# Optimization experiments

Measured on AMD Instinct MI355X. Metric: run time of the kernel, lower is better.

Reference implementation:

```python
import jax, jax.numpy as jnp
import numpy as np

KS = (3, 3)   # kernel_size
ST = (1, 1)   # stride
PD = (1, 1)   # padding
EPS = 1e-5


def unfold(x):
    """im2col matching torch.nn.Unfold: [B,C,H,W] -> [B, C*kh*kw, L] with (c,kh,kw) channel order, L row-major."""
    kh, kw = KS; sh, sw = ST; ph, pw = PD
    x = jnp.pad(x, ((0, 0), (0, 0), (ph, ph), (pw, pw)))
    B, C, H, W = x.shape
    Ho = (H - kh) // sh + 1
    Wo = (W - kw) // sw + 1
    I = (jnp.arange(Ho) * sh)[:, None, None, None] + jnp.arange(kh)[None, :, None, None]
    J = (jnp.arange(Wo) * sw)[None, None, :, None] + jnp.arange(kw)[None, None, None, :]
    p = x[:, :, I, J]  # [B, C, Ho, kh, Wo, kw]
    return p.transpose(0, 1, 3, 5, 2, 4).reshape(B, C * kh * kw, Ho * Wo)


def fold(cols, x_shape):
    """torch.nn.Fold is exactly the adjoint of Unfold (overlap-add)."""
    _, vjp = jax.vjp(unfold, jnp.zeros(x_shape, cols.dtype))
    return vjp(cols)[0]


def setup_inputs() -> dict:
    key = jax.random.key(0)
    k = jax.random.split(key, 6)
    B, C, H, W = 16, 64, 64, 64
    Cout, K = 64, KS[0] * KS[1]
    return {
        "x_mag": jax.random.uniform(k[0], (B, C, H, W), jnp.float32),
        "x_ang": jax.random.normal(k[1], (B, C, H, W), jnp.float32),
        "w_mag": jax.random.uniform(k[2], (C, K), jnp.float32),
        "w_ang": jax.random.uniform(k[3], (C, K), jnp.float32),
        "w1": jax.random.uniform(k[4], (C, K), jnp.float32),
        "w2": jax.random.uniform(k[5], (Cout, C), jnp.float32),
    }


def reference(x_mag, x_ang, w_mag, w_ang, w1, w2):
    B, C, H, W = x_mag.shape
    K = KS[0] * KS[1]
    Cout = w2.shape[0]
    Ho = (H + 2 * PD[0] - KS[0]) // ST[0] + 1
    Wo = (W + 2 * PD[1] - KS[1]) // ST[1] + 1

    # outer layer: unfold, mix with normalized weights, fold back (overlap-add)
    nws_mag = w_mag ** 2 / jnp.sum(w_mag ** 2)   # _normalize_weights_squared
    nw_ang = w_ang / jnp.sum(w_ang ** 2)         # _normalize_weights
    cm = unfold(x_mag).reshape(B, C, K, -1) + nws_mag[None, :, :, None]
    ca = unfold(x_ang).reshape(B, C, K, -1) * nw_ang[None, :, :, None]
    fm = fold(cm.reshape(B, C * K, -1), (B, C, H, W))
    fa = fold(ca.reshape(B, C * K, -1), (B, C, H, W))

    # helper: second unfold + weighted Frechet-mean reduction
    tbm = unfold(fm).reshape(B, C, K, -1)  # [B,C,K,L]
    tba = unfold(fa).reshape(B, C, K, -1)
    wmm1 = w1 ** 2 / jnp.sum(w1 ** 2, axis=1, keepdims=True)  # row-normalized
    wmm2 = w2 ** 2 / jnp.sum(w2 ** 2, axis=1, keepdims=True)
    wma1 = w1 ** 2 / jnp.sum(w1 ** 2)                          # globally normalized
    wma2 = w2 ** 2 / jnp.sum(w2 ** 2)

    m1 = jnp.einsum('bckl,ck->bcl', jnp.log(tbm + EPS), wmm1)
    out_mag = jnp.exp(jnp.einsum('bcl,oc->bol', m1, wmm2)).reshape(B, Cout, Ho, Wo)
    a1 = jnp.einsum('bckl,ck->bcl', tba, wma1)
    out_ang = jnp.einsum('bcl,oc->bol', a1, wma2).reshape(B, Cout, Ho, Wo)

    # from_polar -> stack (real, imag) on axis 1
    return jnp.stack([out_mag * jnp.cos(out_ang), out_mag * jnp.sin(out_ang)], axis=1)
```

## Files before the change

### kernel.cpp

```cpp
#include <hip/hip_runtime.h>
#include <math.h>

#define NB 16
#define NC 64
#define NL 4096
#define EPSF 1e-5f
#define LOG_EPSF -11.512925464970229f
#define CC 4
#define NCHUNK 16

#define WS_W2T   0
#define WS_RHO   4096
#define WS_SMAG  4160
#define WS_TANG  4736
#define WS_IS12  5312

typedef float f32x2 __attribute__((ext_vector_type(2)));

#define FMA16(ACC, MV, W) \
  (ACC)[0].x = fmaf((MV).x,(W).x,(ACC)[0].x); (ACC)[0].y = fmaf((MV).y,(W).x,(ACC)[0].y); \
  (ACC)[0].z = fmaf((MV).z,(W).x,(ACC)[0].z); (ACC)[0].w = fmaf((MV).w,(W).x,(ACC)[0].w); \
  (ACC)[1].x = fmaf((MV).x,(W).y,(ACC)[1].x); (ACC)[1].y = fmaf((MV).y,(W).y,(ACC)[1].y); \
  (ACC)[1].z = fmaf((MV).z,(W).y,(ACC)[1].z); (ACC)[1].w = fmaf((MV).w,(W).y,(ACC)[1].w); \
  (ACC)[2].x = fmaf((MV).x,(W).z,(ACC)[2].x); (ACC)[2].y = fmaf((MV).y,(W).z,(ACC)[2].y); \
  (ACC)[2].z = fmaf((MV).z,(W).z,(ACC)[2].z); (ACC)[2].w = fmaf((MV).w,(W).z,(ACC)[2].w); \
  (ACC)[3].x = fmaf((MV).x,(W).w,(ACC)[3].x); (ACC)[3].y = fmaf((MV).y,(W).w,(ACC)[3].y); \
  (ACC)[3].z = fmaf((MV).z,(W).w,(ACC)[3].z); (ACC)[3].w = fmaf((MV).w,(W).w,(ACC)[3].w);

__global__ __launch_bounds__(256) void prep_kernel(
    const float* __restrict__ wm, const float* __restrict__ wa,
    const float* __restrict__ w1, const float* __restrict__ w2,
    float* __restrict__ ws)
{
    __shared__ float r2s[64];
    __shared__ float red[3][4];
    const int tid  = threadIdx.x;
    const int lane = tid & 63;
    const int wv   = tid >> 6;

    if (tid < 64) {
        float s = 0.f;
        for (int c = 0; c < 64; ++c) { float v = w2[tid * 64 + c]; s = fmaf(v, v, s); }
        r2s[tid] = s;
    }
    float p0 = 0.f, p1 = 0.f, p2 = 0.f;
    {
        float v;
        v = wm[tid]; p0 += v * v;  v = wm[tid + 256]; p0 += v * v;
        v = wa[tid]; p1 += v * v;  v = wa[tid + 256]; p1 += v * v;
        v = w1[tid]; p2 += v * v;  v = w1[tid + 256]; p2 += v * v;
        if (tid < 64) {
            v = wm[tid + 512]; p0 += v * v;
            v = wa[tid + 512]; p1 += v * v;
            v = w1[tid + 512]; p2 += v * v;
        }
    }
    #pragma unroll
    for (int s = 32; s; s >>= 1) {
        p0 += __shfl_down(p0, s); p1 += __shfl_down(p1, s); p2 += __shfl_down(p2, s);
    }
    if (lane == 0) { red[0][wv] = p0; red[1][wv] = p1; red[2][wv] = p2; }
    __syncthreads();
    const float s_wm2 = red[0][0] + red[0][1] + red[0][2] + red[0][3];
    const float s_wa2 = red[1][0] + red[1][1] + red[1][2] + red[1][3];
    const float s_w12 = red[2][0] + red[2][1] + red[2][2] + red[2][3];

    const int c0 = blockIdx.x * 4;
    {
        int c = c0 + (tid >> 6), o = tid & 63;
        float v = w2[o * 64 + c];
        ws[WS_W2T + c * 64 + o] = v * v / r2s[o];
    }

    if (blockIdx.x == 0) {
        if (tid < 64) {
            float s22 = 0.f;
            #pragma unroll
            for (int o = 0; o < 64; ++o) s22 += r2s[o];
            ws[WS_RHO + tid] = r2s[tid] / s22;

            const int c = tid;
            float nm[9], na[9];
            const float inv_m = 1.f / s_wm2, inv_a = 1.f / s_wa2;
            #pragma unroll
            for (int k = 0; k < 9; ++k) {
                float v = wm[c * 9 + k];
                nm[k] = v * v * inv_m;
                na[k] = wa[c * 9 + k] * inv_a;
            }
            #pragma unroll
            for (int ci_ = 0; ci_ < 3; ++ci_) {
                #pragma unroll
                for (int cj = 0; cj < 3; ++cj) {
                    float sm = 0.f, sa = 0.f;
                    #pragma unroll
                    for (int ki = 0; ki < 3; ++ki) {
                        bool vi = (ci_ == 0) ? (ki < 2) : ((ci_ == 2) ? (ki > 0) : true);
                        if (!vi) continue;
                        #pragma unroll
                        for (int kj = 0; kj < 3; ++kj) {
                            bool vj = (cj == 0) ? (kj < 2) : ((cj == 2) ? (kj > 0) : true);
                            if (!vj) continue;
                            sm += nm[ki * 3 + kj];
                            sa += na[ki * 3 + kj];
                        }
                    }
                    ws[WS_SMAG + c * 9 + ci_ * 3 + cj] = sm;
                    ws[WS_TANG + c * 9 + ci_ * 3 + cj] = sa;
                }
            }
        }
        if (tid == 0) ws[WS_IS12] = 1.f / s_w12;
    }
}

__global__ __launch_bounds__(256, 2) void fused_kernel(
    const float* __restrict__ x_mag, const float* __restrict__ x_ang,
    const float* __restrict__ w1, const float* __restrict__ ws,
    float* __restrict__ out)
{
    __shared__ __align__(16) float lf2[CC][4][144];
    __shared__ __align__(16) float m1r[2][CC][2][64];
    __shared__ __align__(16) float a1r[2][CC][2][64];
    __shared__ float smag_s[576], tang_s[576];

    const int tid  = threadIdx.x;
    const int lane = tid & 63;
    const int wv   = tid >> 6;

    const int bid = (blockIdx.x & 7) * 64 + (blockIdx.x >> 3);
    const int b  = bid >> 5;
    const int i0 = (bid & 31) * 2;

    const int sr = lane >> 4;
    const int j4 = lane & 15;
    const int ir = i0 - 1 + sr;
    const bool ok = ((unsigned)ir < 64u);
    const int irc = ok ? ir : 0;
    const int ci = (ir == 0) ? 0 : ((ir == 63) ? 2 : 1);
    const int kL = ci * 3 + 0, kC = ci * 3 + 1, kR = ci * 3 + 2;
    const float ni = (ci == 1) ? 3.f : 2.f;
    const float nCt = 3.f * ni;
    const float n0 = (j4 == 0)  ? 2.f * ni : nCt;
    const float n3 = (j4 == 15) ? 2.f * ni : nCt;

    const float* spm = x_mag + ((size_t)(b * NC + wv) * NL + irc * 64 + j4 * 4);
    const float* spa = x_ang + ((size_t)(b * NC + wv) * NL + irc * 64 + j4 * 4);

    float4 pfm = *(const float4*)spm;
    float4 pfa = *(const float4*)spa;

    const int mrr = tid >> 7;
    const int o0  = ((tid >> 4) & 7) * 8;
    const int l0  = (tid & 15) * 4;

    const float* w2t_g = ws + WS_W2T;
    const float inv_s12 = ws[WS_IS12];

    {
        float4 v0 = ((const float4*)(ws + WS_SMAG))[tid & 127];
        if (tid < 128) *(float4*)&smag_s[tid * 4] = v0;
        else           *(float4*)&tang_s[(tid - 128) * 4] = v0;
        if (tid < 16)  smag_s[512 + tid * 4 + 0] = ws[WS_SMAG + 512 + tid * 4 + 0],
                       smag_s[512 + tid * 4 + 1] = ws[WS_SMAG + 512 + tid * 4 + 1],
                       smag_s[512 + tid * 4 + 2] = ws[WS_SMAG + 512 + tid * 4 + 2],
                       smag_s[512 + tid * 4 + 3] = ws[WS_SMAG + 512 + tid * 4 + 3];
        else if (tid < 32) {
            int t = tid - 16;
            tang_s[512 + t * 4 + 0] = ws[WS_TANG + 512 + t * 4 + 0];
            tang_s[512 + t * 4 + 1] = ws[WS_TANG + 512 + t * 4 + 1];
            tang_s[512 + t * 4 + 2] = ws[WS_TANG + 512 + t * 4 + 2];
            tang_s[512 + t * 4 + 3] = ws[WS_TANG + 512 + t * 4 + 3];
        }
    }
    if (j4 == 0)  { lf2[wv][sr][6]   = LOG_EPSF; lf2[wv][sr][7]   = 0.f; }
    if (j4 == 15) { lf2[wv][sr][136] = LOG_EPSF; lf2[wv][sr][137] = 0.f; }
    if (!ok) {
        float4 s4; s4.x = LOG_EPSF; s4.y = 0.f; s4.z = LOG_EPSF; s4.w = 0.f;
        *(float4*)&lf2[wv][sr][8 + 8 * j4]  = s4;
        *(float4*)&lf2[wv][sr][12 + 8 * j4] = s4;
    }
    __syncthreads();

    float4 accm[8], acca[8];
    #pragma unroll
    for (int oi = 0; oi < 8; ++oi) {
        accm[oi].x = accm[oi].y = accm[oi].z = accm[oi].w = 0.f;
        acca[oi].x = acca[oi].y = acca[oi].z = acca[oi].w = 0.f;
    }

    auto do_matmul = [&](int chm, int pp) {
        const int c0 = chm * CC;
        #pragma unroll
        for (int cc = 0; cc < CC; ++cc) {
            const float* wg = w2t_g + (size_t)(c0 + cc) * 64 + o0;
            float4 w0_ = *(const float4*)(wg);
            float4 w1_ = *(const float4*)(wg + 4);
            float4 mv  = *(const float4*)&m1r[pp][cc][mrr][l0];
            float4 av  = *(const float4*)&a1r[pp][cc][mrr][l0];
            FMA16((&accm[0]), mv, w0_);
            FMA16((&accm[4]), mv, w1_);
            FMA16((&acca[0]), av, w0_);
            FMA16((&acca[4]), av, w1_);
        }
    };

    #pragma unroll 2
    for (int ch = 0; ch < NCHUNK; ++ch) {
        const int p = ch & 1;
        const int cg = ch * CC + wv;

        const int cgu = __builtin_amdgcn_readfirstlane(cg);
        const float* w1row = w1 + cgu * 9;
        float q[9];
        #pragma unroll
        for (int k = 0; k < 9; ++k) q[k] = w1row[k];

        if (ok) {
            float sC = smag_s[cg * 9 + kC], tC = tang_s[cg * 9 + kC];
            float s0 = (j4 == 0)  ? smag_s[cg * 9 + kL] : sC;
            float s3 = (j4 == 15) ? smag_s[cg * 9 + kR] : sC;
            float t0 = (j4 == 0)  ? tang_s[cg * 9 + kL] : tC;
            float t3 = (j4 == 15) ? tang_s[cg * 9 + kR] : tC;
            float4 v0, v1;
            v0.x = __logf(fmaf(n0,  pfm.x, s0) + EPSF);
            v0.y = pfa.x * t0;
            v0.z = __logf(fmaf(nCt, pfm.y, sC) + EPSF);
            v0.w = pfa.y * tC;
            v1.x = __logf(fmaf(nCt, pfm.z, sC) + EPSF);
            v1.y = pfa.z * tC;
            v1.z = __logf(fmaf(n3,  pfm.w, s3) + EPSF);
            v1.w = pfa.w * t3;
            *(float4*)&lf2[wv][sr][8 + 8 * j4]  = v0;
            *(float4*)&lf2[wv][sr][12 + 8 * j4] = v1;
        }

        if (ch + 1 < NCHUNK) {
            pfm = *(const float4*)(spm + (size_t)(ch + 1) * CC * NL);
            pfa = *(const float4*)(spa + (size_t)(ch + 1) * CC * NL);
        }

        if (ch > 0) do_matmul(ch - 1, p ^ 1);

        #pragma unroll
        for (int k = 0; k < 9; ++k) q[k] = q[k] * q[k];
        const float r1c = ((q[0] + q[1]) + (q[2] + q[3])) + ((q[4] + q[5]) + (q[6] + q[7])) + q[8];
        const float inv_r1 = 1.f / r1c;
        f32x2 q2[9];
        #pragma unroll
        for (int k = 0; k < 9; ++k) { q2[k].x = q[k]; q2[k].y = q[k]; }

        {
            f32x2 a0; a0.x = 0.f; a0.y = 0.f;
            f32x2 a1; a1.x = 0.f; a1.y = 0.f;
            #pragma unroll
            for (int r_ = 0; r_ < 4; ++r_) {
                const float* rp = &lf2[wv][r_][0];
                f32x2 v0 = *(const f32x2*)(rp + 2 * lane + 6);
                f32x2 v1 = *(const f32x2*)(rp + 2 * lane + 8);
                f32x2 v2 = *(const f32x2*)(rp + 2 * lane + 10);
                if (r_ < 3) {
                    a0 = __builtin_elementwise_fma(q2[r_ * 3 + 0], v0, a0);
                    a0 = __builtin_elementwise_fma(q2[r_ * 3 + 1], v1, a0);
                    a0 = __builtin_elementwise_fma(q2[r_ * 3 + 2], v2, a0);
                }
                if (r_ > 0) {
                    const int ki = r_ - 1;
                    a1 = __builtin_elementwise_fma(q2[ki * 3 + 0], v0, a1);
                    a1 = __builtin_elementwise_fma(q2[ki * 3 + 1], v1, a1);
                    a1 = __builtin_elementwise_fma(q2[ki * 3 + 2], v2, a1);
                }
            }
            m1r[p][wv][0][lane] = a0.x * inv_r1;
            a1r[p][wv][0][lane] = a0.y * inv_s12;
            m1r[p][wv][1][lane] = a1.x * inv_r1;
            a1r[p][wv][1][lane] = a1.y * inv_s12;
        }
        __syncthreads();
    }
    do_matmul(NCHUNK - 1, 1);

    {
        const float4 rh0 = *(const float4*)(ws + WS_RHO + o0);
        const float4 rh1 = *(const float4*)(ws + WS_RHO + o0 + 4);
        acca[0].x *= rh0.x; acca[0].y *= rh0.x; acca[0].z *= rh0.x; acca[0].w *= rh0.x;
        acca[1].x *= rh0.y; acca[1].y *= rh0.y; acca[1].z *= rh0.y; acca[1].w *= rh0.y;
        acca[2].x *= rh0.z; acca[2].y *= rh0.z; acca[2].z *= rh0.z; acca[2].w *= rh0.z;
        acca[3].x *= rh0.w; acca[3].y *= rh0.w; acca[3].z *= rh0.w; acca[3].w *= rh0.w;
        acca[4].x *= rh1.x; acca[4].y *= rh1.x; acca[4].z *= rh1.x; acca[4].w *= rh1.x;
        acca[5].x *= rh1.y; acca[5].y *= rh1.y; acca[5].z *= rh1.y; acca[5].w *= rh1.y;
        acca[6].x *= rh1.z; acca[6].y *= rh1.z; acca[6].z *= rh1.z; acca[6].w *= rh1.z;
        acca[7].x *= rh1.w; acca[7].y *= rh1.w; acca[7].z *= rh1.w; acca[7].w *= rh1.w;
    }

    #pragma unroll
    for (int oi = 0; oi < 8; ++oi) {
        float4 am = accm[oi], aa = acca[oi];
        float4 oc, os;
        float ex;
        ex = __expf(am.x); oc.x = ex * __cosf(aa.x); os.x = ex * __sinf(aa.x);
        ex = __expf(am.y); oc.y = ex * __cosf(aa.y); os.y = ex * __sinf(aa.y);
        ex = __expf(am.z); oc.z = ex * __cosf(aa.z); os.z = ex * __sinf(aa.z);
        ex = __expf(am.w); oc.w = ex * __cosf(aa.w); os.w = ex * __sinf(aa.w);
        size_t gi = ((size_t)(b * 2) * NC + o0 + oi) * NL + (size_t)(i0 + mrr) * 64 + l0;
        *(float4*)&out[gi] = oc;
        *(float4*)&out[gi + (size_t)NC * NL] = os;
    }
}

extern "C" void kernel_launch(void* const* d_in, const int* in_sizes, int n_in,
                              void* d_out, int out_size, void* d_ws, size_t ws_size,
                              hipStream_t stream) {
    const float* x_mag = (const float*)d_in[0];
    const float* x_ang = (const float*)d_in[1];
    const float* w_mag = (const float*)d_in[2];
    const float* w_ang = (const float*)d_in[3];
    const float* w1    = (const float*)d_in[4];
    const float* w2    = (const float*)d_in[5];
    float* out = (float*)d_out;
    float* ws  = (float*)d_ws;

    prep_kernel<<<16, 256, 0, stream>>>(w_mag, w_ang, w1, w2, ws);
    fused_kernel<<<NB * 32, 256, 0, stream>>>(x_mag, x_ang, w1, ws, out);
}
```

Baseline: 41.22 us.

## Process one output row per block and precompute normalized w1 weights in prep

Each block now handles a single output row instead of two, doubling the grid to 1024 blocks, halving accumulator registers and raising the launch-bounds occupancy target to 4 blocks per SM. The prep kernel now precomputes the row- and globally-normalized squared w1 weights as interleaved pairs, so the main loop no longer squares, sums and divides them per chunk. The previous chunk's matmul is moved before the log/scale stage. The cost is that each block reloads three input rows to produce one output row, so the 3-row halo is read 3x instead of 2x per output row, and a quarter of lanes idle during staging.

```diff
diff --git a/kernel.cpp b/kernel.cpp
--- a/kernel.cpp
+++ b/kernel.cpp
@@ -11,9 +11,8 @@
 
 #define WS_W2T   0
 #define WS_RHO   4096
-#define WS_SMAG  4160
-#define WS_TANG  4736
-#define WS_IS12  5312
+#define WS_CLS   4160
+#define WS_WQ2   5312
 
 typedef float f32x2 __attribute__((ext_vector_type(2)));
 
@@ -105,37 +104,45 @@
                             sa += na[ki * 3 + kj];
                         }
                     }
-                    ws[WS_SMAG + c * 9 + ci_ * 3 + cj] = sm;
-                    ws[WS_TANG + c * 9 + ci_ * 3 + cj] = sa;
+                    ws[WS_CLS + c * 9 + ci_ * 3 + cj] = sm;
+                    ws[WS_CLS + 576 + c * 9 + ci_ * 3 + cj] = sa;
                 }
             }
-        }
-        if (tid == 0) ws[WS_IS12] = 1.f / s_w12;
+            float q[9]; float r1c = 0.f;
+            #pragma unroll
+            for (int k = 0; k < 9; ++k) { float v = w1[c * 9 + k]; q[k] = v * v; r1c += q[k]; }
+            const float inv_r = 1.f / r1c, inv_s = 1.f / s_w12;
+            #pragma unroll
+            for (int k = 0; k < 9; ++k) {
+                ws[WS_WQ2 + c * 18 + 2 * k]     = q[k] * inv_r;
+                ws[WS_WQ2 + c * 18 + 2 * k + 1] = q[k] * inv_s;
+            }
+        }
     }
 }
 
-__global__ __launch_bounds__(256, 2) void fused_kernel(
+__global__ __launch_bounds__(256, 4) void fused_kernel(
     const float* __restrict__ x_mag, const float* __restrict__ x_ang,
-    const float* __restrict__ w1, const float* __restrict__ ws,
-    float* __restrict__ out)
+    const float* __restrict__ ws, float* __restrict__ out)
 {
-    __shared__ __align__(16) float lf2[CC][4][144];
-    __shared__ __align__(16) float m1r[2][CC][2][64];
-    __shared__ __align__(16) float a1r[2][CC][2][64];
-    __shared__ float smag_s[576], tang_s[576];
+    __shared__ __align__(16) float lf2[CC][3][144];
+    __shared__ __align__(16) float m1r[2][CC][64];
+    __shared__ __align__(16) float a1r[2][CC][64];
+    __shared__ __align__(16) float cls_s[1152];
 
     const int tid  = threadIdx.x;
     const int lane = tid & 63;
     const int wv   = tid >> 6;
 
-    const int bid = (blockIdx.x & 7) * 64 + (blockIdx.x >> 3);
-    const int b  = bid >> 5;
-    const int i0 = (bid & 31) * 2;
+    const int bid = (blockIdx.x & 7) * 128 + (blockIdx.x >> 3);
+    const int b  = bid >> 6;
+    const int iy = bid & 63;
 
     const int sr = lane >> 4;
     const int j4 = lane & 15;
-    const int ir = i0 - 1 + sr;
-    const bool ok = ((unsigned)ir < 64u);
+    const bool act = (sr < 3);
+    const int ir = iy - 1 + sr;
+    const bool ok = act && ((unsigned)ir < 64u);
     const int irc = ok ? ir : 0;
     const int ci = (ir == 0) ? 0 : ((ir == 63) ? 2 : 1);
     const int kL = ci * 3 + 0, kC = ci * 3 + 1, kR = ci * 3 + 2;
@@ -147,44 +154,30 @@
     const float* spm = x_mag + ((size_t)(b * NC + wv) * NL + irc * 64 + j4 * 4);
     const float* spa = x_ang + ((size_t)(b * NC + wv) * NL + irc * 64 + j4 * 4);
 
-    float4 pfm = *(const float4*)spm;
-    float4 pfa = *(const float4*)spa;
-
-    const int mrr = tid >> 7;
-    const int o0  = ((tid >> 4) & 7) * 8;
-    const int l0  = (tid & 15) * 4;
-
+    float4 pfm, pfa;
+    if (act) { pfm = *(const float4*)spm; pfa = *(const float4*)spa; }
+
+    const int o0 = (tid >> 4) * 4;
+    const int l0 = (tid & 15) * 4;
     const float* w2t_g = ws + WS_W2T;
-    const float inv_s12 = ws[WS_IS12];
-
-    {
-        float4 v0 = ((const float4*)(ws + WS_SMAG))[tid & 127];
-        if (tid < 128) *(float4*)&smag_s[tid * 4] = v0;
-        else           *(float4*)&tang_s[(tid - 128) * 4] = v0;
-        if (tid < 16)  smag_s[512 + tid * 4 + 0] = ws[WS_SMAG + 512 + tid * 4 + 0],
-                       smag_s[512 + tid * 4 + 1] = ws[WS_SMAG + 512 + tid * 4 + 1],
-                       smag_s[512 + tid * 4 + 2] = ws[WS_SMAG + 512 + tid * 4 + 2],
-                       smag_s[512 + tid * 4 + 3] = ws[WS_SMAG + 512 + tid * 4 + 3];
-        else if (tid < 32) {
-            int t = tid - 16;
-            tang_s[512 + t * 4 + 0] = ws[WS_TANG + 512 + t * 4 + 0];
-            tang_s[512 + t * 4 + 1] = ws[WS_TANG + 512 + t * 4 + 1];
-            tang_s[512 + t * 4 + 2] = ws[WS_TANG + 512 + t * 4 + 2];
-            tang_s[512 + t * 4 + 3] = ws[WS_TANG + 512 + t * 4 + 3];
-        }
-    }
-    if (j4 == 0)  { lf2[wv][sr][6]   = LOG_EPSF; lf2[wv][sr][7]   = 0.f; }
-    if (j4 == 15) { lf2[wv][sr][136] = LOG_EPSF; lf2[wv][sr][137] = 0.f; }
-    if (!ok) {
-        float4 s4; s4.x = LOG_EPSF; s4.y = 0.f; s4.z = LOG_EPSF; s4.w = 0.f;
-        *(float4*)&lf2[wv][sr][8 + 8 * j4]  = s4;
-        *(float4*)&lf2[wv][sr][12 + 8 * j4] = s4;
+
+    for (int t = tid; t < 288; t += 256)
+        ((float4*)cls_s)[t] = ((const float4*)(ws + WS_CLS))[t];
+
+    if (act) {
+        if (j4 == 0)  { lf2[wv][sr][6]   = LOG_EPSF; lf2[wv][sr][7]   = 0.f; }
+        if (j4 == 15) { lf2[wv][sr][136] = LOG_EPSF; lf2[wv][sr][137] = 0.f; }
+        if (!ok) {
+            float4 s4; s4.x = LOG_EPSF; s4.y = 0.f; s4.z = LOG_EPSF; s4.w = 0.f;
+            *(float4*)&lf2[wv][sr][8 + 8 * j4]  = s4;
+            *(float4*)&lf2[wv][sr][12 + 8 * j4] = s4;
+        }
     }
     __syncthreads();
 
-    float4 accm[8], acca[8];
+    float4 accm[4], acca[4];
     #pragma unroll
-    for (int oi = 0; oi < 8; ++oi) {
+    for (int oi = 0; oi < 4; ++oi) {
         accm[oi].x = accm[oi].y = accm[oi].z = accm[oi].w = 0.f;
         acca[oi].x = acca[oi].y = acca[oi].z = acca[oi].w = 0.f;
     }
@@ -194,14 +187,11 @@
         #pragma unroll
         for (int cc = 0; cc < CC; ++cc) {
             const float* wg = w2t_g + (size_t)(c0 + cc) * 64 + o0;
-            float4 w0_ = *(const float4*)(wg);
-            float4 w1_ = *(const float4*)(wg + 4);
-            float4 mv  = *(const float4*)&m1r[pp][cc][mrr][l0];
-            float4 av  = *(const float4*)&a1r[pp][cc][mrr][l0];
-            FMA16((&accm[0]), mv, w0_);
-            FMA16((&accm[4]), mv, w1_);
-            FMA16((&acca[0]), av, w0_);
-            FMA16((&acca[4]), av, w1_);
+            float4 w_ = *(const float4*)wg;
+            float4 mv = *(const float4*)&m1r[pp][cc][l0];
+            float4 av = *(const float4*)&a1r[pp][cc][l0];
+            FMA16(accm, mv, w_);
+            FMA16(acca, av, w_);
         }
     };
 
@@ -211,17 +201,19 @@
         const int cg = ch * CC + wv;
 
         const int cgu = __builtin_amdgcn_readfirstlane(cg);
-        const float* w1row = w1 + cgu * 9;
-        float q[9];
+        const f32x2* qp = (const f32x2*)(ws + WS_WQ2 + cgu * 18);
+        f32x2 q2[9];
         #pragma unroll
-        for (int k = 0; k < 9; ++k) q[k] = w1row[k];
+        for (int k = 0; k < 9; ++k) q2[k] = qp[k];
+
+        if (ch > 0) do_matmul(ch - 1, p ^ 1);
 
         if (ok) {
-            float sC = smag_s[cg * 9 + kC], tC = tang_s[cg * 9 + kC];
-            float s0 = (j4 == 0)  ? smag_s[cg * 9 + kL] : sC;
-            float s3 = (j4 == 15) ? smag_s[cg * 9 + kR] : sC;
-            float t0 = (j4 == 0)  ? tang_s[cg * 9 + kL] : tC;
-            float t3 = (j4 == 15) ? tang_s[cg * 9 + kR] : tC;
+            float sC = cls_s[cg * 9 + kC],       tC = cls_s[576 + cg * 9 + kC];
+            float s0 = (j4 == 0)  ? cls_s[cg * 9 + kL] : sC;
+            float s3 = (j4 == 15) ? cls_s[cg * 9 + kR] : sC;
+            float t0 = (j4 == 0)  ? cls_s[576 + cg * 9 + kL] : tC;
+            float t3 = (j4 == 15) ? cls_s[576 + cg * 9 + kR] : tC;
             float4 v0, v1;
             v0.x = __logf(fmaf(n0,  pfm.x, s0) + EPSF);
             v0.y = pfa.x * t0;
@@ -235,66 +227,40 @@
             *(float4*)&lf2[wv][sr][12 + 8 * j4] = v1;
         }
 
-        if (ch + 1 < NCHUNK) {
+        if (act && (ch + 1 < NCHUNK)) {
             pfm = *(const float4*)(spm + (size_t)(ch + 1) * CC * NL);
             pfa = *(const float4*)(spa + (size_t)(ch + 1) * CC * NL);
         }
 
-        if (ch > 0) do_matmul(ch - 1, p ^ 1);
-
-        #pragma unroll
-        for (int k = 0; k < 9; ++k) q[k] = q[k] * q[k];
-        const float r1c = ((q[0] + q[1]) + (q[2] + q[3])) + ((q[4] + q[5]) + (q[6] + q[7])) + q[8];
-        const float inv_r1 = 1.f / r1c;
-        f32x2 q2[9];
-        #pragma unroll
-        for (int k = 0; k < 9; ++k) { q2[k].x = q[k]; q2[k].y = q[k]; }
-
         {
             f32x2 a0; a0.x = 0.f; a0.y = 0.f;
-            f32x2 a1; a1.x = 0.f; a1.y = 0.f;
-            #pragma unroll
-            for (int r_ = 0; r_ < 4; ++r_) {
+            #pragma unroll
+            for (int r_ = 0; r_ < 3; ++r_) {
                 const float* rp = &lf2[wv][r_][0];
                 f32x2 v0 = *(const f32x2*)(rp + 2 * lane + 6);
                 f32x2 v1 = *(const f32x2*)(rp + 2 * lane + 8);
                 f32x2 v2 = *(const f32x2*)(rp + 2 * lane + 10);
-                if (r_ < 3) {
-                    a0 = __builtin_elementwise_fma(q2[r_ * 3 + 0], v0, a0);
-                    a0 = __builtin_elementwise_fma(q2[r_ * 3 + 1], v1, a0);
-                    a0 = __builtin_elementwise_fma(q2[r_ * 3 + 2], v2, a0);
-                }
-                if (r_ > 0) {
-                    const int ki = r_ - 1;
-                    a1 = __builtin_elementwise_fma(q2[ki * 3 + 0], v0, a1);
-                    a1 = __builtin_elementwise_fma(q2[ki * 3 + 1], v1, a1);
-                    a1 = __builtin_elementwise_fma(q2[ki * 3 + 2], v2, a1);
-                }
-            }
-            m1r[p][wv][0][lane] = a0.x * inv_r1;
-            a1r[p][wv][0][lane] = a0.y * inv_s12;
-            m1r[p][wv][1][lane] = a1.x * inv_r1;
-            a1r[p][wv][1][lane] = a1.y * inv_s12;
+                a0 = __builtin_elementwise_fma(q2[r_ * 3 + 0], v0, a0);
+                a0 = __builtin_elementwise_fma(q2[r_ * 3 + 1], v1, a0);
+                a0 = __builtin_elementwise_fma(q2[r_ * 3 + 2], v2, a0);
+            }
+            m1r[p][wv][lane] = a0.x;
+            a1r[p][wv][lane] = a0.y;
         }
         __syncthreads();
     }
     do_matmul(NCHUNK - 1, 1);
 
     {
-        const float4 rh0 = *(const float4*)(ws + WS_RHO + o0);
-        const float4 rh1 = *(const float4*)(ws + WS_RHO + o0 + 4);
-        acca[0].x *= rh0.x; acca[0].y *= rh0.x; acca[0].z *= rh0.x; acca[0].w *= rh0.x;
-        acca[1].x *= rh0.y; acca[1].y *= rh0.y; acca[1].z *= rh0.y; acca[1].w *= rh0.y;
-        acca[2].x *= rh0.z; acca[2].y *= rh0.z; acca[2].z *= rh0.z; acca[2].w *= rh0.z;
-        acca[3].x *= rh0.w; acca[3].y *= rh0.w; acca[3].z *= rh0.w; acca[3].w *= rh0.w;
-        acca[4].x *= rh1.x; acca[4].y *= rh1.x; acca[4].z *= rh1.x; acca[4].w *= rh1.x;
-        acca[5].x *= rh1.y; acca[5].y *= rh1.y; acca[5].z *= rh1.y; acca[5].w *= rh1.y;
-        acca[6].x *= rh1.z; acca[6].y *= rh1.z; acca[6].z *= rh1.z; acca[6].w *= rh1.z;
-        acca[7].x *= rh1.w; acca[7].y *= rh1.w; acca[7].z *= rh1.w; acca[7].w *= rh1.w;
+        const float4 rh = *(const float4*)(ws + WS_RHO + o0);
+        acca[0].x *= rh.x; acca[0].y *= rh.x; acca[0].z *= rh.x; acca[0].w *= rh.x;
+        acca[1].x *= rh.y; acca[1].y *= rh.y; acca[1].z *= rh.y; acca[1].w *= rh.y;
+        acca[2].x *= rh.z; acca[2].y *= rh.z; acca[2].z *= rh.z; acca[2].w *= rh.z;
+        acca[3].x *= rh.w; acca[3].y *= rh.w; acca[3].z *= rh.w; acca[3].w *= rh.w;
     }
 
     #pragma unroll
-    for (int oi = 0; oi < 8; ++oi) {
+    for (int oi = 0; oi < 4; ++oi) {
         float4 am = accm[oi], aa = acca[oi];
         float4 oc, os;
         float ex;
@@ -302,7 +268,7 @@
         ex = __expf(am.y); oc.y = ex * __cosf(aa.y); os.y = ex * __sinf(aa.y);
         ex = __expf(am.z); oc.z = ex * __cosf(aa.z); os.z = ex * __sinf(aa.z);
         ex = __expf(am.w); oc.w = ex * __cosf(aa.w); os.w = ex * __sinf(aa.w);
-        size_t gi = ((size_t)(b * 2) * NC + o0 + oi) * NL + (size_t)(i0 + mrr) * 64 + l0;
+        size_t gi = ((size_t)(b * 2) * NC + o0 + oi) * NL + (size_t)iy * 64 + l0;
         *(float4*)&out[gi] = oc;
         *(float4*)&out[gi + (size_t)NC * NL] = os;
     }
@@ -321,5 +287,5 @@
     float* ws  = (float*)d_ws;
 
     prep_kernel<<<16, 256, 0, stream>>>(w_mag, w_ang, w1, w2, ws);
-    fused_kernel<<<NB * 32, 256, 0, stream>>>(x_mag, x_ang, w1, ws, out);
+    fused_kernel<<<NB * 64, 256, 0, stream>>>(x_mag, x_ang, ws, out);
 }
```

Result: no change. 40.61 us (-1.5%).
